# Kernel tuning notes

Measured on AMD Instinct MI355X. Metric: run time of the kernel, lower is better.

The kernel has to match this reference:

```python
import jax, jax.numpy as jnp
import numpy as np
from jax import lax

SQRT2 = 1.4142135623730951
EPS_VAR = 1e-10
BN_EPS = 1e-5

# --- LR-net probabilistic ternary-weight conv math (Shayer et al. local reparameterization) ---
# Weight w in {-1,0,+1}: p0 = sigmoid(alpha) = P(w=0); p1 = (1-p0)*sigmoid(betta) = P(w=+1).
# E[w] = p1 - p_{-1} = 2*p1 - (1-p0);  E[w^2] = 1-p0;  Var[w] = E[w^2] - E[w]^2.

def _conv(x, w, stride):
    return lax.conv_general_dilated(x, w, (stride, stride), [(1, 1), (1, 1)],
                                    dimension_numbers=("NCHW", "OIHW", "NCHW"))

def ternary_stats(alpha, betta):
    p0 = jax.nn.sigmoid(alpha)
    p1 = (1.0 - p0) * jax.nn.sigmoid(betta)
    e_w = 2.0 * p1 - (1.0 - p0)
    e_w2 = 1.0 - p0
    return e_w, e_w2 - e_w * e_w, e_w2

def lrconv(x, alpha, betta, bias, stride):
    # LRnetConv2d (train mode): deterministic input tensor -> Gaussian (mean, var) output
    e_w, var_w, _ = ternary_stats(alpha, betta)
    m = _conv(x, e_w, stride) + bias[None, :, None, None]
    v = _conv(x * x, var_w, stride)
    return m, v

def lrconv_ver2(m, v, alpha, betta, bias, stride):
    # LRnetConv2d_ver2: Gaussian (m,v) input passed through probabilistic sign,
    # then ternary conv with analytic mean/variance propagation.
    sigma = jnp.sqrt(v + EPS_VAR)
    e_x = lax.erf(m / (sigma * SQRT2))       # E[sign(x)] = 2*Phi(m/sigma)-1; E[sign(x)^2] = 1
    e_w, var_w, e_w2 = ternary_stats(alpha, betta)
    m_out = _conv(e_x, e_w, stride) + bias[None, :, None, None]
    # Var = sum E[w^2]*E[x^2] - E[w]^2*E[x]^2  (zero padding -> deterministic 0 inputs)
    v_out = _conv(jnp.ones_like(e_x), e_w2, stride) - _conv(e_x * e_x, e_w * e_w, stride)
    return m_out, v_out

def batchnorm(x, gamma, beta):
    mu = x.mean(axis=(0, 2, 3), keepdims=True)
    var = x.var(axis=(0, 2, 3), keepdims=True)
    return gamma[None, :, None, None] * (x - mu) * lax.rsqrt(var + BN_EPS) + beta[None, :, None, None]


def setup_inputs() -> dict:
    key = jax.random.key(0)
    ks = iter(jax.random.split(key, 40))
    B = 256
    d = {}
    d["x"] = jax.random.normal(next(ks), (B, 3, 32, 32), jnp.float32)
    shapes = [(128, 3, 3, 3), (128, 128, 3, 3), (256, 128, 3, 3),
              (256, 256, 3, 3), (512, 256, 3, 3), (512, 512, 3, 3)]
    for i, s in enumerate(shapes, start=1):
        d[f"a{i}"] = jax.random.normal(next(ks), s, jnp.float32) * 0.1
        d[f"b{i}"] = jax.random.normal(next(ks), s, jnp.float32) * 0.1
        d[f"c{i}"] = jnp.zeros((s[0],), jnp.float32)
    d["g3"] = jnp.ones((256,), jnp.float32); d["be3"] = jnp.zeros((256,), jnp.float32)
    d["g6"] = jnp.ones((512,), jnp.float32); d["be6"] = jnp.zeros((512,), jnp.float32)
    d["fc1_w"] = jax.random.normal(next(ks), (1024, 8192), jnp.float32) * (1.0 / np.sqrt(8192))
    d["fc1_b"] = jnp.zeros((1024,), jnp.float32)
    d["fc2_w"] = jax.random.normal(next(ks), (10, 1024), jnp.float32) * (1.0 / np.sqrt(1024))
    d["fc2_b"] = jnp.zeros((10,), jnp.float32)
    d["eps3"] = jax.random.normal(next(ks), (B, 256, 16, 16), jnp.float32)
    d["eps6"] = jax.random.normal(next(ks), (B, 512, 4, 4), jnp.float32)
    return d


def reference(x, a1, b1, c1, a2, b2, c2, a3, b3, c3, a4, b4, c4, a5, b5, c5, a6, b6, c6,
              g3, be3, g6, be6, fc1_w, fc1_b, fc2_w, fc2_b, eps3, eps6):
    m, v = lrconv(x, a1, b1, c1, 1)                  # 32x32, 128
    m, v = lrconv_ver2(m, v, a2, b2, c2, 2)          # 16x16, 128
    m, v = lrconv_ver2(m, v, a3, b3, c3, 1)          # 16x16, 256
    h = m + jnp.sqrt(v + EPS_VAR) * eps3             # output_sample=True
    h = jax.nn.relu(batchnorm(h, g3, be3))
    m, v = lrconv(h, a4, b4, c4, 2)                  # 8x8, 256
    m, v = lrconv_ver2(m, v, a5, b5, c5, 1)          # 8x8, 512
    m, v = lrconv_ver2(m, v, a6, b6, c6, 2)          # 4x4, 512
    h = m + jnp.sqrt(v + EPS_VAR) * eps6             # output_sample=True
    h = jax.nn.relu(batchnorm(h, g6, be6))
    h = h.reshape(h.shape[0], -1)                    # [B, 8192]
    h = jax.nn.relu(h @ fc1_w.T + fc1_b)
    return h @ fc2_w.T + fc2_b                       # [B, 10] logits
```

## Files before the change

### kernel.cpp

```cpp
#include <hip/hip_runtime.h>
#include <hip/hip_bf16.h>
#include <math.h>

#define EPSV 1e-10f
#define BNEPS 1e-5f
#define INV_SQRT2 0.70710678118654752440f

typedef __attribute__((ext_vector_type(8))) short short8;
typedef __attribute__((ext_vector_type(4))) float f32x4;
typedef _Float16 half8 __attribute__((ext_vector_type(8)));

__device__ __forceinline__ unsigned short f2h(float f) {
    _Float16 h = (_Float16)f;
    return __builtin_bit_cast(unsigned short, h);
}
__device__ __forceinline__ float h2f(unsigned short u) {
    _Float16 h = __builtin_bit_cast(_Float16, u);
    return (float)h;
}

__global__ void prep_w(const float* __restrict__ a, const float* __restrict__ b,
                       float* __restrict__ WA, float* __restrict__ WB, int n) {
    for (int i = blockIdx.x * blockDim.x + threadIdx.x; i < n; i += gridDim.x * blockDim.x) {
        float p0 = 1.f / (1.f + expf(-a[i]));
        float sb = 1.f / (1.f + expf(-b[i]));
        float p1 = (1.f - p0) * sb;
        float ew = 2.f * p1 - (1.f - p0);
        float ew2 = 1.f - p0;
        WA[i] = ew;
        WB[i] = ew2 - ew * ew;
    }
}

__global__ void prep_packL1(const float* __restrict__ wa, const float* __restrict__ wb,
                            unsigned short* __restrict__ pk) {
    int idx = blockIdx.x * 256 + threadIdx.x;
    if (idx >= 1024) return;
    int lane = idx & 63;
    int mf = (idx >> 6) & 7;
    int cv = idx >> 9;
    int co = mf * 16 + (lane & 15);
    int k0 = (lane >> 4) * 8;
    const float* src = (cv ? wb : wa) + co * 27;
    unsigned int o[4] = {0, 0, 0, 0};
#pragma unroll
    for (int j = 0; j < 8; j++) {
        int k = k0 + j;
        if (k < 27) {
            unsigned int h = f2h(src[k]);
            o[j >> 1] |= h << ((j & 1) * 16);
        }
    }
    uint4 v; v.x = o[0]; v.y = o[1]; v.z = o[2]; v.w = o[3];
    *(uint4*)(pk + (long)idx * 8) = v;
}

__global__ void prep_pack(const float* __restrict__ a, const float* __restrict__ b,
                          unsigned short* __restrict__ pk, int Ci, int Co, int ver2, int total) {
    int idx = blockIdx.x * 256 + threadIdx.x;
    if (idx >= total) return;
    int lane = idx & 63;
    int MFg = Co >> 4, NCH = Ci >> 5;
    int mfch = idx >> 6;
    int mf = mfch % MFg;
    int chpos = mfch / MFg;
    int ch = chpos % NCH;
    int pos = chpos / NCH;
    int co = mf * 16 + (lane & 15);
    int cib = ch * 32 + (lane >> 4) * 8;
    unsigned int wa[4], wb[4];
#pragma unroll
    for (int j = 0; j < 8; j++) {
        long s = ((long)co * Ci + cib + j) * 9 + pos;
        float p0 = 1.f / (1.f + expf(-a[s]));
        float sb = 1.f / (1.f + expf(-b[s]));
        float p1 = (1.f - p0) * sb;
        float ew = 2.f * p1 - (1.f - p0);
        float ew2 = 1.f - p0;
        unsigned int ha = f2h(ew);
        unsigned int hb = f2h(ver2 ? ew * ew : ew2 - ew * ew);
        if (j & 1) { wa[j >> 1] |= ha << 16; wb[j >> 1] |= hb << 16; }
        else       { wa[j >> 1] = ha;        wb[j >> 1] = hb; }
    }
    long b0 = (((long)(0 * 9 + pos) * NCH + ch) * MFg + mf) * 64 + lane;
    long b1 = (((long)(1 * 9 + pos) * NCH + ch) * MFg + mf) * 64 + lane;
    uint4 va; va.x = wa[0]; va.y = wa[1]; va.z = wa[2]; va.w = wa[3];
    uint4 vb; vb.x = wb[0]; vb.y = wb[1]; vb.z = wb[2]; vb.w = wb[3];
    *(uint4*)(pk + b0 * 8) = va;
    *(uint4*)(pk + b1 * 8) = vb;
}

__global__ void prep_s(const float* __restrict__ alpha, float* __restrict__ s, int Ci) {
    int co = blockIdx.x;
    int lane = threadIdx.x;
    float acc[9];
#pragma unroll
    for (int k = 0; k < 9; k++) acc[k] = 0.f;
    for (int ci = lane; ci < Ci; ci += 64) {
        const float* p = alpha + ((long)co * Ci + ci) * 9;
#pragma unroll
        for (int k = 0; k < 9; k++) acc[k] += 1.f / (1.f + expf(p[k]));
    }
#pragma unroll
    for (int k = 0; k < 9; k++) {
        for (int off = 32; off > 0; off >>= 1) acc[k] += __shfl_down(acc[k], off);
    }
    if (lane == 0) {
#pragma unroll
        for (int k = 0; k < 9; k++) s[co * 9 + k] = acc[k];
    }
}

__global__ void prep_ones(const float* __restrict__ ssum, float* __restrict__ og,
                          int Co, int Hout, int Wout, int Hin, int Win, int stride, int total) {
    int idx = blockIdx.x * 256 + threadIdx.x;
    if (idx >= total) return;
    int x = idx % Wout, y = (idx / Wout) % Hout, co = idx / (Wout * Hout);
    float s = 0.f;
    for (int ky = 0; ky < 3; ky++) {
        int yi = stride * y - 1 + ky;
        if (yi < 0 || yi >= Hin) continue;
        for (int kx = 0; kx < 3; kx++) {
            int xi = stride * x - 1 + kx;
            if (xi < 0 || xi >= Win) continue;
            s += ssum[co * 9 + ky * 3 + kx];
        }
    }
    og[idx] = s;
}

__global__ void prep_fc1(const float* __restrict__ W, unsigned short* __restrict__ pk) {
    int idx = blockIdx.x * 256 + threadIdx.x;
    int lane = idx & 63;
    int mf = (idx >> 6) & 63;
    int kt = idx >> 12;
    int o = mf * 16 + (lane & 15);
    long k = (long)kt * 32 + (lane >> 4) * 8;
    const float* src = W + (long)o * 8192 + k;
    float4 f0 = *(const float4*)src;
    float4 f1 = *(const float4*)(src + 4);
    uint4 v;
    v.x = (unsigned)f2h(f0.x) | ((unsigned)f2h(f0.y) << 16);
    v.y = (unsigned)f2h(f0.z) | ((unsigned)f2h(f0.w) << 16);
    v.z = (unsigned)f2h(f1.x) | ((unsigned)f2h(f1.y) << 16);
    v.w = (unsigned)f2h(f1.z) | ((unsigned)f2h(f1.w) << 16);
    *(uint4*)(pk + (long)idx * 8) = v;
}

__global__ void l1_im2col(const float* __restrict__ x, unsigned short* __restrict__ cols) {
    int n = blockIdx.x * 256 + threadIdx.x;
    int b = n >> 10, y = (n >> 5) & 31, xx = n & 31;
    unsigned int o[16];
#pragma unroll
    for (int i = 0; i < 16; i++) o[i] = 0;
#pragma unroll
    for (int ci = 0; ci < 3; ci++)
#pragma unroll
    for (int ky = 0; ky < 3; ky++) {
        int yy = y - 1 + ky;
        if (yy < 0 || yy > 31) continue;
#pragma unroll
        for (int kx = 0; kx < 3; kx++) {
            int xc = xx - 1 + kx;
            if (xc < 0 || xc > 31) continue;
            float v = x[((b * 3 + ci) * 32 + yy) * 32 + xc];
            int k = ci * 9 + ky * 3 + kx;
            o[k >> 1] |= ((unsigned int)f2h(v)) << ((k & 1) * 16);
        }
    }
    uint4* dst = (uint4*)(cols + (long)n * 32);
    uint4 v0; v0.x = o[0];  v0.y = o[1];  v0.z = o[2];  v0.w = o[3];
    uint4 v1; v1.x = o[4];  v1.y = o[5];  v1.z = o[6];  v1.w = o[7];
    uint4 v2; v2.x = o[8];  v2.y = o[9];  v2.z = o[10]; v2.w = o[11];
    uint4 v3; v3.x = o[12]; v3.y = o[13]; v3.z = o[14]; v3.w = o[15];
    dst[0] = v0; dst[1] = v1; dst[2] = v2; dst[3] = v3;
}

__global__ __launch_bounds__(512) void conv1_mfma(const unsigned short* __restrict__ cols,
        const unsigned short* __restrict__ Wp, const float* __restrict__ bias,
        unsigned short* __restrict__ out) {
    constexpr int LINE = 80;
    constexpr int TSTR = 136;
    __shared__ char lds[128 * TSTR * 2];
    const int tid = threadIdx.x, lane = tid & 63, wv = tid >> 6;
    const int wm = wv & 1, wn = wv >> 1;
    const int g = lane >> 4, ln = lane & 15;
    const long n0 = (long)blockIdx.x * 128;

    for (int i = tid; i < 128 * 4; i += 512) {
        int r = i >> 2, c = i & 3;
        uint4 v = *(const uint4*)(cols + (n0 + r) * 32 + c * 8);
        *(uint4*)(lds + r * LINE + c * 16) = v;
    }
    __syncthreads();

    half8 af[2][4];
#pragma unroll
    for (int cv = 0; cv < 2; cv++)
#pragma unroll
    for (int m = 0; m < 4; m++)
        af[cv][m] = *(const half8*)(Wp + ((long)((cv * 8 + wm * 4 + m) * 64 + lane)) * 8);

    f32x4 accA[4][2], accB[4][2];
#pragma unroll
    for (int m = 0; m < 4; m++)
#pragma unroll
    for (int nf = 0; nf < 2; nf++) {
        accA[m][nf] = (f32x4){0.f, 0.f, 0.f, 0.f};
        accB[m][nf] = (f32x4){0.f, 0.f, 0.f, 0.f};
    }
#pragma unroll
    for (int nf = 0; nf < 2; nf++) {
        int r = wn * 32 + nf * 16 + ln;
        half8 b1 = *(const half8*)(lds + r * LINE + g * 16);
        half8 b2 = b1 * b1;
#pragma unroll
        for (int m = 0; m < 4; m++) {
            accA[m][nf] = __builtin_amdgcn_mfma_f32_16x16x32_f16(af[0][m], b1, accA[m][nf], 0, 0, 0);
            accB[m][nf] = __builtin_amdgcn_mfma_f32_16x16x32_f16(af[1][m], b2, accB[m][nf], 0, 0, 0);
        }
    }
    __syncthreads();
#pragma unroll
    for (int m = 0; m < 4; m++) {
        int cob = (wm * 4 + m) * 16 + g * 4;
#pragma unroll
        for (int nf = 0; nf < 2; nf++) {
            int nl = wn * 32 + nf * 16 + ln;
            unsigned int pk2[2];
#pragma unroll
            for (int r = 0; r < 4; r++) {
                float mm = accA[m][nf][r] + bias[cob + r];
                float vv = accB[m][nf][r];
                unsigned int hv = f2h(erff(mm * rsqrtf(vv + EPSV) * INV_SQRT2));
                if (r & 1) pk2[r >> 1] |= hv << 16; else pk2[r >> 1] = hv;
            }
            *(unsigned int*)(lds + (nl * TSTR + cob) * 2) = pk2[0];
            *(unsigned int*)(lds + (nl * TSTR + cob) * 2 + 4) = pk2[1];
        }
    }
    __syncthreads();
    for (int i = tid; i < 128 * 16; i += 512) {
        int nl = i >> 4, c8 = (i & 15) * 8;
        uint4 v = *(const uint4*)(lds + (nl * TSTR + c8) * 2);
        *(uint4*)(out + (n0 + nl) * 128 + c8) = v;
    }
}

template<int Ci, int Hin, int Win, int Co, int Hout, int Wout, int STRIDE,
         int ROWS, int IPB, int NTILE, int CHUNK, int MTILE, int MODE>
__global__ __launch_bounds__(512) void conv_mfma(
    const unsigned short* __restrict__ in,
    const unsigned short* __restrict__ wpk,
    const float* __restrict__ bias,
    const float* __restrict__ ones_g,
    const float* __restrict__ epsb,
    void* __restrict__ outp)
{
    constexpr int BLK = 512;
    constexpr int PROWS = STRIDE * (ROWS - 1) + 3;
    constexpr int PW = Win + 2;
    constexpr int POS = IPB * PROWS * PW;
    constexpr int NCH32 = Ci / 32;
    constexpr int NCHL = Ci / CHUNK;
    constexpr int KS = CHUNK / 32;
    constexpr int MFg = Co / 16;
    constexpr int NF = NTILE / 16;
    constexpr int WMF = MTILE / 32;
    constexpr int WNF = NF / 4;
    constexpr int CT = Co / MTILE;
    constexpr int RG = Hout / ROWS;
    constexpr int LINE = CHUNK * 2 + 16;
    constexpr int TSTR = MTILE + 8;
    constexpr int PASSN = (NTILE < 128) ? NTILE : 128;
    constexpr int NPASS = (MODE == 4) ? 0 : NTILE / PASSN;
    constexpr int STAGE_B = POS * LINE;
    constexpr int TR_B = (MODE == 4) ? 0 : PASSN * TSTR * 2;
    constexpr int LDS_B = STAGE_B > TR_B ? STAGE_B : TR_B;
    static_assert(8 % CT == 0, "ct swizzle");
    static_assert(WNF * 4 == NF, "wnf");
    static_assert(WMF * 32 == MTILE, "wmf");
    static_assert(NCHL * CHUNK == Ci, "chunk");
    static_assert(LDS_B <= 65536, "lds");
    __shared__ char lds[LDS_B];

    const int tid = threadIdx.x;
    const int lane = tid & 63;
    const int wv = tid >> 6;
    const int wm = wv & 1, wn = wv >> 1;
    const int g = lane >> 4, ln = lane & 15;

    const int bid = blockIdx.x;
    const int xcd = bid & 7;
    constexpr int XPC = 8 / CT;
    const int ct = xcd % CT;
    const int nt = (bid >> 3) * XPC + xcd / CT;
    const int b0 = (nt / RG) * IPB;
    const int y0 = (nt % RG) * ROWS;

    int pbase[WNF];
#pragma unroll
    for (int nf = 0; nf < WNF; nf++) {
        int n = (wn * WNF + nf) * 16 + ln;
        int img = n / (ROWS * Wout);
        int rem = n % (ROWS * Wout);
        int yr = rem / Wout, xo = rem % Wout;
        pbase[nf] = (img * PROWS + STRIDE * yr) * PW + STRIDE * xo;
    }

    f32x4 accA[WMF][WNF], accB[WMF][WNF];
#pragma unroll
    for (int mf = 0; mf < WMF; mf++)
#pragma unroll
    for (int nf = 0; nf < WNF; nf++) {
        accA[mf][nf] = (f32x4){0.f, 0.f, 0.f, 0.f};
        accB[mf][nf] = (f32x4){0.f, 0.f, 0.f, 0.f};
    }

    const unsigned short* wbase = wpk + ((long)(ct * (MTILE / 16) + wm * WMF) * 64 + lane) * 8;

    for (int ch = 0; ch < NCHL; ch++) {
        for (int i = tid; i < POS * (CHUNK / 8); i += BLK) {
            int p = i / (CHUNK / 8), c = i % (CHUNK / 8);
            int img = p / (PROWS * PW);
            int r = p % (PROWS * PW);
            int prow = r / PW, px = r % PW;
            int yin = STRIDE * y0 - 1 + prow;
            int xin = px - 1;
            uint4 v; v.x = 0; v.y = 0; v.z = 0; v.w = 0;
            if (yin >= 0 && yin < Hin && xin >= 0 && xin < Win) {
                long a = (((long)(b0 + img) * Hin + yin) * Win + xin) * Ci + ch * CHUNK + c * 8;
                v = *(const uint4*)(in + a);
            }
            *(uint4*)(lds + p * LINE + c * 16) = v;
        }
        __syncthreads();
#pragma unroll 3
        for (int pos = 0; pos < 9; pos++) {
            const int ky = pos / 3, kx = pos % 3;
#pragma unroll
            for (int ks = 0; ks < KS; ks++) {
                const int ch32 = ch * KS + ks;
                half8 af[2][WMF];
#pragma unroll
                for (int cv = 0; cv < 2; cv++)
#pragma unroll
                for (int mf = 0; mf < WMF; mf++)
                    af[cv][mf] = *(const half8*)(wbase +
                        ((long)(((cv * 9 + pos) * NCH32 + ch32) * MFg + mf)) * 512);
#pragma unroll
                for (int nf = 0; nf < WNF; nf++) {
                    int po = (pbase[nf] + ky * PW + kx) * LINE + ks * 64 + g * 16;
                    half8 b1 = *(const half8*)(lds + po);
                    half8 b2 = b1 * b1;
#pragma unroll
                    for (int mf = 0; mf < WMF; mf++) {
                        accA[mf][nf] = __builtin_amdgcn_mfma_f32_16x16x32_f16(af[0][mf], b1, accA[mf][nf], 0, 0, 0);
                        accB[mf][nf] = __builtin_amdgcn_mfma_f32_16x16x32_f16(af[1][mf], b2, accB[mf][nf], 0, 0, 0);
                    }
                }
            }
        }
        __syncthreads();
    }

    if constexpr (MODE == 4) {
        unsigned short* out = (unsigned short*)outp;
#pragma unroll
        for (int mf = 0; mf < WMF; mf++) {
            int co = ct * MTILE + (wm * WMF + mf) * 16 + g * 4;
#pragma unroll
            for (int nf = 0; nf < WNF; nf++) {
                int n = (wn * WNF + nf) * 16 + ln;
                int img = n / (ROWS * Wout), rem = n % (ROWS * Wout);
                int y = y0 + rem / Wout, x = rem % Wout;
                int b = b0 + img;
#pragma unroll
                for (int r = 0; r < 4; r++) {
                    int c = co + r;
                    float m = accA[mf][nf][r] + bias[c];
                    float v = ones_g[(c * Hout + y) * Wout + x] - accB[mf][nf][r];
                    long oi = (((long)b * Co + c) * Hout + y) * Wout + x;
                    out[oi] = f2h(m + sqrtf(v + EPSV) * epsb[oi]);
                }
            }
        }
    } else {
        unsigned short* out = (unsigned short*)outp;
#pragma unroll
        for (int pass = 0; pass < NPASS; pass++) {
            __syncthreads();
#pragma unroll
            for (int mf = 0; mf < WMF; mf++) {
                int cob = (wm * WMF + mf) * 16 + g * 4;
                int cg = ct * MTILE + cob;
#pragma unroll
                for (int nf = 0; nf < WNF; nf++) {
                    int nb = (wn * WNF + nf) * 16;
                    if (nb < pass * PASSN || nb >= (pass + 1) * PASSN) continue;
                    int n = nb + ln;
                    int img = n / (ROWS * Wout), rem = n % (ROWS * Wout);
                    int y = y0 + rem / Wout, x = rem % Wout;
                    int b = b0 + img;
                    unsigned int pk2[2];
#pragma unroll
                    for (int r = 0; r < 4; r++) {
                        int c = cg + r;
                        float m = accA[mf][nf][r] + bias[c];
                        float val;
                        if constexpr (MODE == 0) {
                            val = erff(m * rsqrtf(accB[mf][nf][r] + EPSV) * INV_SQRT2);
                        } else if constexpr (MODE == 1) {
                            float v = ones_g[(c * Hout + y) * Wout + x] - accB[mf][nf][r];
                            val = erff(m * rsqrtf(v + EPSV) * INV_SQRT2);
                        } else {
                            float v = ones_g[(c * Hout + y) * Wout + x] - accB[mf][nf][r];
                            float ev = epsb[(((long)b * Co + c) * Hout + y) * Wout + x];
                            val = m + sqrtf(v + EPSV) * ev;
                        }
                        unsigned int hv = f2h(val);
                        if (r & 1) pk2[r >> 1] |= hv << 16; else pk2[r >> 1] = hv;
                    }
                    int nl = n - pass * PASSN;
                    *(unsigned int*)(lds + (nl * TSTR + cob) * 2) = pk2[0];
                    *(unsigned int*)(lds + (nl * TSTR + cob) * 2 + 4) = pk2[1];
                }
            }
            __syncthreads();
            for (int i = tid; i < PASSN * (MTILE / 8); i += BLK) {
                int nl = i / (MTILE / 8);
                int n = pass * PASSN + nl;
                int c8 = (i % (MTILE / 8)) * 8;
                int img = n / (ROWS * Wout), rem = n % (ROWS * Wout);
                int y = y0 + rem / Wout, x = rem % Wout;
                int b = b0 + img;
                uint4 val = *(const uint4*)(lds + (nl * TSTR + c8) * 2);
                long oa = (((long)b * Hout + y) * Wout + x) * Co + ct * MTILE + c8;
                *(uint4*)(out + oa) = val;
            }
        }
    }
}

__global__ void bn_part_nhwc(const unsigned short* __restrict__ h, float* __restrict__ part,
                             int C, int rpc) {
    int c = threadIdx.x;
    long r0 = (long)blockIdx.x * rpc;
    float s = 0.f, s2 = 0.f;
    for (int r = 0; r < rpc; r++) {
        float v = h2f(h[(r0 + r) * C + c]);
        s += v; s2 += v * v;
    }
    part[(long)blockIdx.x * 2 * C + c] = s;
    part[(long)blockIdx.x * 2 * C + C + c] = s2;
}

__global__ void bn_part_nchw(const unsigned short* __restrict__ h, float* __restrict__ part,
                             int ipc) {
    int c = threadIdx.x;
    int b0 = blockIdx.x * ipc;
    float s = 0.f, s2 = 0.f;
    for (int b = 0; b < ipc; b++) {
        const unsigned short* p = h + ((long)(b0 + b) * 512 + c) * 16;
        uint4 v0 = *(const uint4*)p;
        uint4 v1 = *(const uint4*)(p + 8);
        unsigned int* vp0 = (unsigned int*)&v0;
        unsigned int* vp1 = (unsigned int*)&v1;
#pragma unroll
        for (int e = 0; e < 4; e++) {
            float a = h2f((unsigned short)(vp0[e] & 0xffffu)), bb = h2f((unsigned short)(vp0[e] >> 16));
            float cc = h2f((unsigned short)(vp1[e] & 0xffffu)), d = h2f((unsigned short)(vp1[e] >> 16));
            s += a + bb + cc + d;
            s2 += a * a + bb * bb + cc * cc + d * d;
        }
    }
    part[(long)blockIdx.x * 1024 + c] = s;
    part[(long)blockIdx.x * 1024 + 512 + c] = s2;
}

__global__ void bn_fin(const float* __restrict__ part, const float* __restrict__ gamma,
                       const float* __restrict__ beta, float* __restrict__ sc,
                       float* __restrict__ sh, int C, int chunks, float invN) {
    int c = blockIdx.x * 256 + threadIdx.x;
    if (c >= C) return;
    float s = 0.f, s2 = 0.f;
    for (int j = 0; j < chunks; j++) {
        s += part[(long)j * 2 * C + c];
        s2 += part[(long)j * 2 * C + C + c];
    }
    float mean = s * invN;
    float var = s2 * invN - mean * mean;
    float k = gamma[c] * rsqrtf(var + BNEPS);
    sc[c] = k;
    sh[c] = beta[c] - mean * k;
}

__global__ void bn_app_nhwc(unsigned short* __restrict__ h, const float* __restrict__ sc,
                            const float* __restrict__ sh) {
    int i = blockIdx.x * 256 + threadIdx.x;
    int cb = (i & 31) * 8;
    uint4 v = *(uint4*)(h + (long)i * 8);
    float4 s0 = *(const float4*)(sc + cb), s1 = *(const float4*)(sc + cb + 4);
    float4 t0 = *(const float4*)(sh + cb), t1 = *(const float4*)(sh + cb + 4);
    float scl[8] = {s0.x, s0.y, s0.z, s0.w, s1.x, s1.y, s1.z, s1.w};
    float shf[8] = {t0.x, t0.y, t0.z, t0.w, t1.x, t1.y, t1.z, t1.w};
    unsigned int* vp = (unsigned int*)&v;
#pragma unroll
    for (int e = 0; e < 4; e++) {
        float lo = h2f((unsigned short)(vp[e] & 0xffffu));
        float hi = h2f((unsigned short)(vp[e] >> 16));
        lo = fmaf(lo, scl[2 * e], shf[2 * e]);     lo = lo > 0.f ? lo : 0.f;
        hi = fmaf(hi, scl[2 * e + 1], shf[2 * e + 1]); hi = hi > 0.f ? hi : 0.f;
        vp[e] = (unsigned int)f2h(lo) | (((unsigned int)f2h(hi)) << 16);
    }
    *(uint4*)(h + (long)i * 8) = v;
}

__global__ void bn_app_nchw(unsigned short* __restrict__ h, const float* __restrict__ sc,
                            const float* __restrict__ sh) {
    int i = blockIdx.x * 256 + threadIdx.x;
    int c = (i >> 1) & 511;
    float k = sc[c], t = sh[c];
    uint4 v = *(uint4*)(h + (long)i * 8);
    unsigned int* vp = (unsigned int*)&v;
#pragma unroll
    for (int e = 0; e < 4; e++) {
        float lo = h2f((unsigned short)(vp[e] & 0xffffu));
        float hi = h2f((unsigned short)(vp[e] >> 16));
        lo = fmaf(lo, k, t); lo = lo > 0.f ? lo : 0.f;
        hi = fmaf(hi, k, t); hi = hi > 0.f ? hi : 0.f;
        vp[e] = (unsigned int)f2h(lo) | (((unsigned int)f2h(hi)) << 16);
    }
    *(uint4*)(h + (long)i * 8) = v;
}

__global__ __launch_bounds__(256) void fc1_mfma(const unsigned short* __restrict__ Ab,
                                                const unsigned short* __restrict__ Wp,
                                                float* __restrict__ pbuf) {
    __shared__ char lds[2 * 64 * 80];
    const int tid = threadIdx.x;
    const int lane = tid & 63;
    const int wv = tid >> 6;
    const int g = lane >> 4, ln = lane & 15;
    const int ot = blockIdx.x, bt = blockIdx.y, s = blockIdx.z;
    const int b0 = bt * 64;
    const int k0g = s * 1024;

    f32x4 acc[2][4];
#pragma unroll
    for (int c = 0; c < 2; c++)
#pragma unroll
    for (int nf = 0; nf < 4; nf++) acc[c][nf] = (f32x4){0.f, 0.f, 0.f, 0.f};

    for (int k0 = 0; k0 < 1024; k0 += 64) {
        __syncthreads();
        for (int i = tid; i < 512; i += 256) {
            int row = i >> 3, kk = (i >> 2) & 1, seg = i & 3;
            uint4 v = *(const uint4*)(Ab + ((long)(b0 + row) * 8192 + k0g + k0 + kk * 32 + seg * 8));
            *(uint4*)(lds + (kk * 64 + row) * 80 + seg * 16) = v;
        }
        __syncthreads();
#pragma unroll
        for (int kk = 0; kk < 2; kk++) {
            int kt = (k0g + k0) / 32 + kk;
            half8 af[2];
#pragma unroll
            for (int c = 0; c < 2; c++) {
                int mf = ot * 8 + wv * 2 + c;
                af[c] = *(const half8*)(Wp + (((long)kt * 64 + mf) * 64 + lane) * 8);
            }
            half8 bf[4];
#pragma unroll
            for (int nf = 0; nf < 4; nf++)
                bf[nf] = *(const half8*)(lds + (kk * 64 + nf * 16 + ln) * 80 + g * 16);
#pragma unroll
            for (int c = 0; c < 2; c++)
#pragma unroll
            for (int nf = 0; nf < 4; nf++)
                acc[c][nf] = __builtin_amdgcn_mfma_f32_16x16x32_f16(af[c], bf[nf], acc[c][nf], 0, 0, 0);
        }
    }
#pragma unroll
    for (int c = 0; c < 2; c++) {
        int o = ot * 128 + (wv * 2 + c) * 16 + g * 4;
#pragma unroll
        for (int nf = 0; nf < 4; nf++) {
            int b = b0 + nf * 16 + ln;
            *(f32x4*)(pbuf + ((long)s * 256 + b) * 1024 + o) = acc[c][nf];
        }
    }
}

__global__ void fc1_reduce(const float* __restrict__ pbuf, const float* __restrict__ bias,
                           float* __restrict__ out) {
    int idx = blockIdx.x * 256 + threadIdx.x;
    float s = 0.f;
#pragma unroll
    for (int j = 0; j < 8; j++) s += pbuf[(long)j * 262144 + idx];
    s += bias[idx & 1023];
    out[idx] = s > 0.f ? s : 0.f;
}

__global__ void fc2_k(const float* __restrict__ A, const float* __restrict__ W,
                      const float* __restrict__ b2, float* __restrict__ out) {
    int bb = blockIdx.x;
    int tid = threadIdx.x;
    float acc[10];
#pragma unroll
    for (int o = 0; o < 10; o++) acc[o] = 0.f;
    const float* arow = A + (long)bb * 1024;
    for (int k = tid; k < 1024; k += 256) {
        float a = arow[k];
#pragma unroll
        for (int o = 0; o < 10; o++) acc[o] = fmaf(a, W[o * 1024 + k], acc[o]);
    }
#pragma unroll
    for (int o = 0; o < 10; o++)
        for (int off = 32; off > 0; off >>= 1) acc[o] += __shfl_down(acc[o], off);
    __shared__ float red[10][4];
    int wid = tid >> 6, lane = tid & 63;
    if (lane == 0) {
#pragma unroll
        for (int o = 0; o < 10; o++) red[o][wid] = acc[o];
    }
    __syncthreads();
    if (tid < 10)
        out[bb * 10 + tid] = red[tid][0] + red[tid][1] + red[tid][2] + red[tid][3] + b2[tid];
}

extern "C" void kernel_launch(void* const* d_in, const int* in_sizes, int n_in,
                              void* d_out, int out_size, void* d_ws, size_t ws_size,
                              hipStream_t stream) {
    const float* x  = (const float*)d_in[0];
    const float* a1 = (const float*)d_in[1];  const float* b1 = (const float*)d_in[2];  const float* c1 = (const float*)d_in[3];
    const float* a2 = (const float*)d_in[4];  const float* b2 = (const float*)d_in[5];  const float* c2 = (const float*)d_in[6];
    const float* a3 = (const float*)d_in[7];  const float* b3 = (const float*)d_in[8];  const float* c3 = (const float*)d_in[9];
    const float* a4 = (const float*)d_in[10]; const float* b4 = (const float*)d_in[11]; const float* c4 = (const float*)d_in[12];
    const float* a5 = (const float*)d_in[13]; const float* b5 = (const float*)d_in[14]; const float* c5 = (const float*)d_in[15];
    const float* a6 = (const float*)d_in[16]; const float* b6 = (const float*)d_in[17]; const float* c6 = (const float*)d_in[18];
    const float* g3 = (const float*)d_in[19]; const float* be3 = (const float*)d_in[20];
    const float* g6 = (const float*)d_in[21]; const float* be6 = (const float*)d_in[22];
    const float* fc1w = (const float*)d_in[23]; const float* fc1b = (const float*)d_in[24];
    const float* fc2w = (const float*)d_in[25]; const float* fc2b = (const float*)d_in[26];
    const float* eps3 = (const float*)d_in[27]; const float* eps6 = (const float*)d_in[28];
    (void)in_sizes; (void)n_in; (void)out_size; (void)ws_size;

    float* w = (float*)d_ws;
    size_t off = 0;
    auto alloc = [&](size_t n) { float* p = w + off; off += n; return p; };
    unsigned short* pk2 = (unsigned short*)alloc(147456);
    unsigned short* pk3 = (unsigned short*)alloc(294912);
    unsigned short* pk4 = (unsigned short*)alloc(589824);
    unsigned short* pk5 = (unsigned short*)alloc(1179648);
    unsigned short* pk6 = (unsigned short*)alloc(2359296);
    unsigned short* pkL1 = (unsigned short*)alloc(4096);
    float* wa1 = alloc(3456); float* wb1 = alloc(3456);
    float* ss2 = alloc(1152); float* ss3 = alloc(2304);
    float* ss5 = alloc(4608); float* ss6 = alloc(4608);
    float* og2 = alloc(32768); float* og3 = alloc(65536);
    float* og5 = alloc(32768); float* og6 = alloc(8192);
    float* part3 = alloc(131072);
    float* part6 = alloc(65536);
    float* sc3 = alloc(256); float* sh3 = alloc(256);
    float* sc6 = alloc(512); float* sh6 = alloc(512);
    float* A  = alloc(16777216);
    float* Bb = alloc(4194304);
    float* Cc = alloc(8388608);
    float* Dd = alloc(2097152);
    float* Ee = alloc(4194304);

    unsigned short* ex1 = (unsigned short*)A;
    unsigned short* pkF = (unsigned short*)A;
    float*          pbuf = A + 4194304;
    unsigned short* ex2 = (unsigned short*)Bb;
    float*          fco = Bb;
    unsigned short* h6b = (unsigned short*)(Bb + 524288);
    unsigned short* colsL1 = (unsigned short*)Cc;
    unsigned short* h3b = (unsigned short*)Cc;
    unsigned short* ex4 = (unsigned short*)Dd;
    unsigned short* ex5 = (unsigned short*)Ee;

    prep_w<<<14, 256, 0, stream>>>(a1, b1, wa1, wb1, 3456);
    prep_packL1<<<4, 256, 0, stream>>>(wa1, wb1, pkL1);
    prep_pack<<<72,  256, 0, stream>>>(a2, b2, pk2, 128, 128, 1, 18432);
    prep_pack<<<144, 256, 0, stream>>>(a3, b3, pk3, 128, 256, 1, 36864);
    prep_pack<<<288, 256, 0, stream>>>(a4, b4, pk4, 256, 256, 0, 73728);
    prep_pack<<<576, 256, 0, stream>>>(a5, b5, pk5, 256, 512, 1, 147456);
    prep_pack<<<1152,256, 0, stream>>>(a6, b6, pk6, 512, 512, 1, 294912);
    prep_s<<<128, 64, 0, stream>>>(a2, ss2, 128);
    prep_s<<<256, 64, 0, stream>>>(a3, ss3, 128);
    prep_s<<<512, 64, 0, stream>>>(a5, ss5, 256);
    prep_s<<<512, 64, 0, stream>>>(a6, ss6, 512);
    prep_ones<<<128, 256, 0, stream>>>(ss2, og2, 128, 16, 16, 32, 32, 2, 32768);
    prep_ones<<<256, 256, 0, stream>>>(ss3, og3, 256, 16, 16, 16, 16, 1, 65536);
    prep_ones<<<128, 256, 0, stream>>>(ss5, og5, 512, 8, 8, 8, 8, 1, 32768);
    prep_ones<<<32,  256, 0, stream>>>(ss6, og6, 512, 4, 4, 8, 8, 2, 8192);

    l1_im2col<<<1024, 256, 0, stream>>>(x, colsL1);
    conv1_mfma<<<2048, 512, 0, stream>>>(colsL1, pkL1, c1, ex1);
    conv_mfma<128,32,32,128,16,16,2, 8,1,128,32,128,1><<<512, 512, 0, stream>>>(ex1, pk2, c2, og2, nullptr, ex2);
    conv_mfma<128,16,16,256,16,16,1, 8,2,256,64,128,3><<<512, 512, 0, stream>>>(ex2, pk3, c3, og3, eps3, h3b);
    prep_fc1<<<4096, 256, 0, stream>>>(fc1w, pkF);
    bn_part_nhwc<<<256, 256, 0, stream>>>(h3b, part3, 256, 256);
    bn_fin<<<1, 256, 0, stream>>>(part3, g3, be3, sc3, sh3, 256, 256, 1.f / 65536.f);
    bn_app_nhwc<<<8192, 256, 0, stream>>>(h3b, sc3, sh3);
    conv_mfma<256,16,16,256, 8, 8,2, 8,1,64,32,128,0><<<512, 512, 0, stream>>>(h3b, pk4, c4, nullptr, nullptr, ex4);
    conv_mfma<256, 8, 8,512, 8, 8,1, 8,2,128,32,128,1><<<512, 512, 0, stream>>>(ex4, pk5, c5, og5, nullptr, ex5);
    conv_mfma<512, 8, 8,512, 4, 4,2, 4,4,64,32,64,4><<<512, 512, 0, stream>>>(ex5, pk6, c6, og6, eps6, h6b);
    bn_part_nchw<<<64, 512, 0, stream>>>(h6b, part6, 4);
    bn_fin<<<2, 256, 0, stream>>>(part6, g6, be6, sc6, sh6, 512, 64, 1.f / 4096.f);
    bn_app_nchw<<<2048, 256, 0, stream>>>(h6b, sc6, sh6);
    fc1_mfma<<<dim3(8, 4, 8), 256, 0, stream>>>(h6b, pkF, pbuf);
    fc1_reduce<<<1024, 256, 0, stream>>>(pbuf, fc1b, fco);
    fc2_k<<<256, 256, 0, stream>>>(fco, fc2w, fc2b, (float*)d_out);
}
```

Measured before the change: 793.4 us.

## Prefetch next input chunk into registers while computing current chunk

The conv kernel's input staging now precomputes the per-thread global source pointers and LDS destinations once, outside the channel-chunk loop. The next chunk's global loads are issued into registers right after the barrier, so their latency overlaps the MFMA work on the current chunk. This costs extra VGPRs for the pointer arrays and the prefetched uint4 values, which may reduce occupancy. Correctness depends on the second barrier at the end of each iteration still guarding the LDS overwrite.

Result: no change. 790.5 us (-0.4%).

```diff
diff --git a/kernel.cpp b/kernel.cpp
--- a/kernel.cpp
+++ b/kernel.cpp
@@ -277,6 +277,8 @@
     constexpr int STAGE_B = POS * LINE;
     constexpr int TR_B = (MODE == 4) ? 0 : PASSN * TSTR * 2;
     constexpr int LDS_B = STAGE_B > TR_B ? STAGE_B : TR_B;
+    constexpr int NV = POS * (CHUNK / 8);
+    constexpr int NLD = (NV + BLK - 1) / BLK;
     static_assert(8 % CT == 0, "ct swizzle");
     static_assert(WNF * 4 == NF, "wnf");
     static_assert(WMF * 32 == MTILE, "wmf");
@@ -308,33 +310,58 @@
         pbase[nf] = (img * PROWS + STRIDE * yr) * PW + STRIDE * xo;
     }
 
-    f32x4 accA[WMF][WNF], accB[WMF][WNF];
-#pragma unroll
-    for (int mf = 0; mf < WMF; mf++)
-#pragma unroll
-    for (int nf = 0; nf < WNF; nf++) {
-        accA[mf][nf] = (f32x4){0.f, 0.f, 0.f, 0.f};
-        accB[mf][nf] = (f32x4){0.f, 0.f, 0.f, 0.f};
-    }
-
-    const unsigned short* wbase = wpk + ((long)(ct * (MTILE / 16) + wm * WMF) * 64 + lane) * 8;
-
-    for (int ch = 0; ch < NCHL; ch++) {
-        for (int i = tid; i < POS * (CHUNK / 8); i += BLK) {
+    const unsigned short* gsrc[NLD];
+    int ldst[NLD];
+#pragma unroll
+    for (int j = 0; j < NLD; j++) {
+        int i = tid + j * BLK;
+        gsrc[j] = nullptr; ldst[j] = 0;
+        if (i < NV) {
             int p = i / (CHUNK / 8), c = i % (CHUNK / 8);
             int img = p / (PROWS * PW);
             int r = p % (PROWS * PW);
             int prow = r / PW, px = r % PW;
             int yin = STRIDE * y0 - 1 + prow;
             int xin = px - 1;
-            uint4 v; v.x = 0; v.y = 0; v.z = 0; v.w = 0;
-            if (yin >= 0 && yin < Hin && xin >= 0 && xin < Win) {
-                long a = (((long)(b0 + img) * Hin + yin) * Win + xin) * Ci + ch * CHUNK + c * 8;
-                v = *(const uint4*)(in + a);
+            ldst[j] = p * LINE + c * 16;
+            if (yin >= 0 && yin < Hin && xin >= 0 && xin < Win)
+                gsrc[j] = in + (((long)(b0 + img) * Hin + yin) * Win + xin) * Ci + c * 8;
+        }
+    }
+
+    f32x4 accA[WMF][WNF], accB[WMF][WNF];
+#pragma unroll
+    for (int mf = 0; mf < WMF; mf++)
+#pragma unroll
+    for (int nf = 0; nf < WNF; nf++) {
+        accA[mf][nf] = (f32x4){0.f, 0.f, 0.f, 0.f};
+        accB[mf][nf] = (f32x4){0.f, 0.f, 0.f, 0.f};
+    }
+
+    const unsigned short* wbase = wpk + ((long)(ct * (MTILE / 16) + wm * WMF) * 64 + lane) * 8;
+
+    uint4 regs[NLD];
+#pragma unroll
+    for (int j = 0; j < NLD; j++) {
+        uint4 v; v.x = 0; v.y = 0; v.z = 0; v.w = 0;
+        if (tid + j * BLK < NV && gsrc[j]) v = *(const uint4*)(gsrc[j]);
+        regs[j] = v;
+    }
+
+    for (int ch = 0; ch < NCHL; ch++) {
+#pragma unroll
+        for (int j = 0; j < NLD; j++)
+            if (tid + j * BLK < NV) *(uint4*)(lds + ldst[j]) = regs[j];
+        __syncthreads();
+        if (ch + 1 < NCHL) {
+#pragma unroll
+            for (int j = 0; j < NLD; j++) {
+                uint4 v; v.x = 0; v.y = 0; v.z = 0; v.w = 0;
+                if (tid + j * BLK < NV && gsrc[j])
+                    v = *(const uint4*)(gsrc[j] + (long)(ch + 1) * CHUNK);
+                regs[j] = v;
             }
-            *(uint4*)(lds + p * LINE + c * 16) = v;
-        }
-        __syncthreads();
+        }
 #pragma unroll 3
         for (int pos = 0; pos < 9; pos++) {
             const int ky = pos / 3, kx = pos % 3;
```
